# Kernel optimization log

Hardware: AMD Instinct MI355X
Metric: run time of the kernel (lower is better)

## Reference

```python
import jax, jax.numpy as jnp
import numpy as np

N = 10000        # nodes
E = 160000       # edges
C = 128          # channel multiplicity (128x0e input)
RBF = 20         # edge_attr_dim
HID = 32         # edge MLP hidden
WN = 3 * C       # tp.weight_numel: 3 uvu paths (0e x Y_l -> l), 128 weights each


def setup_inputs() -> dict:
    key = jax.random.key(0)
    ks = jax.random.split(key, 12)
    f = lambda k, s, sc=1.0: jax.random.normal(k, s, jnp.float32) * sc
    return {
        "node_feat": f(ks[0], (N, C)),
        "edge_attr": f(ks[1], (E, RBF)),
        "edge_rsh": f(ks[2], (E, 9)),
        "edge_index": jax.random.randint(ks[3], (2, E), 0, N),
        # mlp_edge_scalar: Linear(2C->32), Linear(32->WN)
        "Ws1": f(ks[4], (2 * C, HID), 1.0 / np.sqrt(2 * C)), "bs1": jnp.zeros((HID,), jnp.float32),
        "Ws2": f(ks[5], (HID, WN), 1.0 / np.sqrt(HID)), "bs2": jnp.zeros((WN,), jnp.float32),
        # mlp_edge_rbf: Linear(20->32), Linear(32->WN)
        "Wr1": f(ks[6], (RBF, HID), 1.0 / np.sqrt(RBF)), "br1": jnp.zeros((HID,), jnp.float32),
        "Wr2": f(ks[7], (HID, WN), 1.0 / np.sqrt(HID)), "br2": jnp.zeros((WN,), jnp.float32),
        "lin2_w0": f(ks[8], (C, C)), "lin2_b0": jnp.zeros((C,), jnp.float32),
        "lin2_w1": f(ks[9], (C, C)),
        "lin2_w2": f(ks[10], (C, C)),
    }


def reference(node_feat, edge_attr, edge_rsh, edge_index,
              Ws1, bs1, Ws2, bs2, Wr1, br1, Wr2, br2,
              lin2_w0, lin2_b0, lin2_w1, lin2_w2):
    src, dst = edge_index[0], edge_index[1]
    xi = node_feat[src]            # [E, C] gathered scalars (center node)
    xj = node_feat[dst]            # [E, C] gathered scalars (neighbor)

    # First-layer branch: inner_dot of pure scalars -> elementwise product;
    # slice [:, C:] is empty, so s0 = concat(x_i scalars, x_j scalars).
    s0 = jnp.concatenate([xi, xj], axis=-1)  # [E, 2C]

    silu = jax.nn.silu
    w_s = silu(s0 @ Ws1 + bs1) @ Ws2 + bs2            # [E, 3C]
    w_r = silu(edge_attr @ Wr1 + br1) @ Wr2 + br2      # [E, 3C]
    tpw = w_s * w_r                                    # gated tensor-product weights

    w0, w1, w2 = tpw[:, :C], tpw[:, C:2 * C], tpw[:, 2 * C:]
    y0, y1, y2 = edge_rsh[:, :1], edge_rsh[:, 1:4], edge_rsh[:, 4:9]

    # uvu tensor product: per edge, per channel u: w_l[u] * x[u] * Y_l[m]
    m0 = (w0 * xj) * y0                                        # [E, C]
    m1 = (w1 * xj)[:, :, None] * y1[:, None, :]                # [E, C, 3]
    m2 = (w2 * xj)[:, :, None] * y2[:, None, :]                # [E, C, 5]
    msg = jnp.concatenate(
        [m0, m1.reshape(-1, 3 * C), m2.reshape(-1, 5 * C)], axis=-1)  # [E, 9C]

    # scatter-add to destination (edge_index[0])
    accu = jax.ops.segment_sum(msg, src, num_segments=node_feat.shape[0])  # [N, 9C]

    # lin_node2: equivariant linear (per-l channel mixing, bias on scalars only)
    a0 = accu[:, :C]
    a1 = accu[:, C:4 * C].reshape(-1, C, 3)
    a2 = accu[:, 4 * C:].reshape(-1, C, 5)
    inv = 1.0 / np.sqrt(C)  # e3nn o3.Linear fan-in normalization
    o0 = a0 @ lin2_w0 * inv + lin2_b0
    o1 = jnp.einsum('ncm,cd->ndm', a1, lin2_w1) * inv
    o2 = jnp.einsum('ncm,cd->ndm', a2, lin2_w2) * inv
    return jnp.concatenate([o0, o1.reshape(-1, 3 * C), o2.reshape(-1, 5 * C)], axis=-1)
```

## Files before the change

kernel.cpp:

```cpp
#include <hip/hip_runtime.h>
#include <hip/hip_bf16.h>
#include <math.h>

#define NN   10000
#define EE   160000
#define CC   128
#define RBFD 20
#define HIDD 32
#define WND  384
#define MROW 1152
#define EPB  64

typedef _Float16 half2_t __attribute__((ext_vector_type(2)));

__device__ __forceinline__ half2_t u2h(unsigned int u)
{
    union { unsigned int u; half2_t h; } c; c.u = u; return c.h;
}
__device__ __forceinline__ unsigned int pack_h2(float a, float b)
{
    union { half2_t h; unsigned int u; } c;
    c.h.x = (_Float16)a; c.h.y = (_Float16)b; return c.u;
}

__device__ __align__(16) float g_proj[(size_t)NN * 64];
__device__ __align__(16) float g_accu[(size_t)NN * MROW];
__device__ __align__(16) uint4 g_wp[3 * 16 * 64];
__device__ int g_deg[NN];
__device__ int g_offs[NN + 1];
__device__ int g_rel[EE];
__device__ int g_ord[EE];

__device__ __forceinline__ float silu_f(float x) { return x / (1.f + __expf(-x)); }

__global__ __launch_bounds__(256) void zero_kernel()
{
    int tid = blockIdx.x * 256 + threadIdx.x;
    if (tid < NN) g_deg[tid] = 0;
    float4* p = reinterpret_cast<float4*>(g_accu);
    float4 z = make_float4(0.f, 0.f, 0.f, 0.f);
    int n4 = NN * MROW / 4;
    for (int i = tid; i < n4; i += gridDim.x * 256) p[i] = z;
}

__global__ __launch_bounds__(192) void pack_kernel(
    const float* __restrict__ Ws2, const float* __restrict__ Wr2)
{
    int tid = threadIdx.x;
    int sec = tid >> 6, l = tid & 63;
    int c0 = sec * 128 + 2 * l;
    #pragma unroll
    for (int q = 0; q < 4; ++q) {
        unsigned int w0[4], w1[4], r0[4], r1[4];
        #pragma unroll
        for (int i = 0; i < 4; ++i) {
            int p = 4 * q + i;
            int b0 = (2 * p) * WND + c0;
            int b1 = (2 * p + 1) * WND + c0;
            w0[i] = pack_h2(Ws2[b0],     Ws2[b1]);
            w1[i] = pack_h2(Ws2[b0 + 1], Ws2[b1 + 1]);
            r0[i] = pack_h2(Wr2[b0],     Wr2[b1]);
            r1[i] = pack_h2(Wr2[b0 + 1], Wr2[b1 + 1]);
        }
        g_wp[((sec * 16 + 0 * 4 + q) * 64) + l] = make_uint4(w0[0], w0[1], w0[2], w0[3]);
        g_wp[((sec * 16 + 1 * 4 + q) * 64) + l] = make_uint4(w1[0], w1[1], w1[2], w1[3]);
        g_wp[((sec * 16 + 2 * 4 + q) * 64) + l] = make_uint4(r0[0], r0[1], r0[2], r0[3]);
        g_wp[((sec * 16 + 3 * 4 + q) * 64) + l] = make_uint4(r1[0], r1[1], r1[2], r1[3]);
    }
}

__global__ __launch_bounds__(256) void hist_kernel(const int* __restrict__ edge_index)
{
    int e = blockIdx.x * 256 + threadIdx.x;
    if (e < EE) g_rel[e] = atomicAdd(&g_deg[edge_index[e]], 1);
}

__global__ __launch_bounds__(256) void scan_kernel()
{
    __shared__ int sP[256];
    int t = threadIdx.x;
    int lo = t * 40, hi = min(lo + 40, NN);
    int sum = 0;
    for (int i = lo; i < hi; ++i) sum += g_deg[i];
    sP[t] = sum;
    __syncthreads();
    for (int off = 1; off < 256; off <<= 1) {
        int v = (t >= off) ? sP[t - off] : 0;
        __syncthreads();
        sP[t] += v;
        __syncthreads();
    }
    int run = sP[t] - sum;
    if (t == 0) g_offs[0] = 0;
    for (int i = lo; i < hi; ++i) { run += g_deg[i]; g_offs[i + 1] = run; }
}

__global__ __launch_bounds__(256) void proj_kernel(
    const float* __restrict__ nf,
    const float* __restrict__ Ws1, const float* __restrict__ bs1,
    const int* __restrict__ edge_index)
{
    __shared__ float sX[16][132];

    int tid = threadIdx.x;
    int nb = blockIdx.x * 16;

    {
        int eg = blockIdx.x * 256 + tid;
        g_ord[g_offs[edge_index[eg]] + g_rel[eg]] = eg;
    }

    #pragma unroll
    for (int i = tid; i < 512; i += 256) {
        int n = i >> 5, k4 = i & 31;
        float4 v = reinterpret_cast<const float4*>(nf + (size_t)(nb + n) * CC)[k4];
        sX[n][k4 * 4 + 0] = v.x;
        sX[n][k4 * 4 + 1] = v.y;
        sX[n][k4 * 4 + 2] = v.z;
        sX[n][k4 * 4 + 3] = v.w;
    }
    __syncthreads();

    int nl = tid >> 4;
    int qd = tid & 15;
    int j0 = (qd & 7) * 4;
    int rbase = (qd >= 8) ? CC : 0;

    float4 acc;
    if (qd < 8) acc = *reinterpret_cast<const float4*>(&bs1[j0]);
    else        acc = make_float4(0.f, 0.f, 0.f, 0.f);

    const float* wb = Ws1 + (size_t)rbase * HIDD + j0;
    #pragma unroll 4
    for (int k = 0; k < CC; ++k) {
        float f = sX[nl][k];
        float4 w = *reinterpret_cast<const float4*>(wb + (size_t)k * HIDD);
        acc.x = fmaf(f, w.x, acc.x);
        acc.y = fmaf(f, w.y, acc.y);
        acc.z = fmaf(f, w.z, acc.z);
        acc.w = fmaf(f, w.w, acc.w);
    }

    float* o = g_proj + (size_t)(nb + nl) * 64 + ((qd >= 8) ? HIDD : 0) + j0;
    *reinterpret_cast<float4*>(o) = acc;
}

template<int K, int YB, int MOFF>
__device__ __forceinline__ void section_pass(
    int sec, int l,
    const float2* __restrict__ nf2,
    const float* __restrict__ bs2, const float* __restrict__ br2,
    const unsigned int (*__restrict__ sH)[36], const float (*__restrict__ sY)[9],
    const int* __restrict__ sSrc, const int* __restrict__ sDst)
{
    const uint4* wt = g_wp + (size_t)sec * 16 * 64 + l;
    uint4 W0q[4], W1q[4], R0q[4], R1q[4];
    #pragma unroll
    for (int q = 0; q < 4; ++q) {
        W0q[q] = wt[(0 * 4 + q) * 64];
        W1q[q] = wt[(1 * 4 + q) * 64];
        R0q[q] = wt[(2 * 4 + q) * 64];
        R1q[q] = wt[(3 * 4 + q) * 64];
    }

    float2 bsv = *reinterpret_cast<const float2*>(&bs2[sec * 128 + 2 * l]);
    float2 brv = *reinterpret_cast<const float2*>(&br2[sec * 128 + 2 * l]);

    float racc0[K], racc1[K];
    #pragma unroll
    for (int k = 0; k < K; ++k) { racc0[k] = 0.f; racc1[k] = 0.f; }
    int cur = sSrc[0];
    float2 xjn = nf2[(size_t)sDst[0] * 64 + l];

    #pragma unroll 2
    for (int ee = 0; ee < EPB; ++ee) {
        int src = sSrc[ee];
        if (src != cur) {
            float* ab = g_accu + (size_t)cur * MROW + MOFF + 2 * l;
            #pragma unroll
            for (int k = 0; k < K; ++k) {
                unsafeAtomicAdd(ab + k * CC,     racc0[k]);
                unsafeAtomicAdd(ab + k * CC + 1, racc1[k]);
                racc0[k] = 0.f; racc1[k] = 0.f;
            }
            cur = src;
        }
        float2 xj = xjn;
        xjn = nf2[(size_t)sDst[(ee + 1) & (EPB - 1)] * 64 + l];
        const uint4* hp = reinterpret_cast<const uint4*>(&sH[ee][0]);
        float as0 = bsv.x, as1 = bsv.y, ar0 = brv.x, ar1 = brv.y;
        #pragma unroll
        for (int q = 0; q < 4; ++q) {
            uint4 hv = hp[q];
            uint4 rv = hp[4 + q];
            as0 = __builtin_amdgcn_fdot2(u2h(hv.x), u2h(W0q[q].x), as0, false);
            as1 = __builtin_amdgcn_fdot2(u2h(hv.x), u2h(W1q[q].x), as1, false);
            as0 = __builtin_amdgcn_fdot2(u2h(hv.y), u2h(W0q[q].y), as0, false);
            as1 = __builtin_amdgcn_fdot2(u2h(hv.y), u2h(W1q[q].y), as1, false);
            as0 = __builtin_amdgcn_fdot2(u2h(hv.z), u2h(W0q[q].z), as0, false);
            as1 = __builtin_amdgcn_fdot2(u2h(hv.z), u2h(W1q[q].z), as1, false);
            as0 = __builtin_amdgcn_fdot2(u2h(hv.w), u2h(W0q[q].w), as0, false);
            as1 = __builtin_amdgcn_fdot2(u2h(hv.w), u2h(W1q[q].w), as1, false);
            ar0 = __builtin_amdgcn_fdot2(u2h(rv.x), u2h(R0q[q].x), ar0, false);
            ar1 = __builtin_amdgcn_fdot2(u2h(rv.x), u2h(R1q[q].x), ar1, false);
            ar0 = __builtin_amdgcn_fdot2(u2h(rv.y), u2h(R0q[q].y), ar0, false);
            ar1 = __builtin_amdgcn_fdot2(u2h(rv.y), u2h(R1q[q].y), ar1, false);
            ar0 = __builtin_amdgcn_fdot2(u2h(rv.z), u2h(R0q[q].z), ar0, false);
            ar1 = __builtin_amdgcn_fdot2(u2h(rv.z), u2h(R1q[q].z), ar1, false);
            ar0 = __builtin_amdgcn_fdot2(u2h(rv.w), u2h(R0q[q].w), ar0, false);
            ar1 = __builtin_amdgcn_fdot2(u2h(rv.w), u2h(R1q[q].w), ar1, false);
        }
        float u0 = as0 * ar0 * xj.x;
        float u1 = as1 * ar1 * xj.y;
        #pragma unroll
        for (int k = 0; k < K; ++k) {
            float yv = sY[ee][YB + k];
            racc0[k] = fmaf(u0, yv, racc0[k]);
            racc1[k] = fmaf(u1, yv, racc1[k]);
        }
    }
    float* ab = g_accu + (size_t)cur * MROW + MOFF + 2 * l;
    #pragma unroll
    for (int k = 0; k < K; ++k) {
        unsafeAtomicAdd(ab + k * CC,     racc0[k]);
        unsafeAtomicAdd(ab + k * CC + 1, racc1[k]);
    }
}

__global__ __launch_bounds__(192, 4) void fused_kernel(
    const float* __restrict__ nf,
    const float* __restrict__ edge_attr,
    const float* __restrict__ edge_rsh,
    const int*   __restrict__ edge_index,
    const float* __restrict__ bs2,
    const float* __restrict__ Wr1, const float* __restrict__ br1,
    const float* __restrict__ br2)
{
    __shared__ unsigned int sH[EPB][36];
    __shared__ float sY[EPB][9];
    __shared__ int   sSrc[EPB], sDst[EPB];

    int tid = threadIdx.x;
    int w = tid / 64;
    int l = tid & 63;
    int p = blockIdx.x * EPB + l;
    int e = g_ord[p];

    if (w == 0) {
        int s = edge_index[e];
        int t = edge_index[EE + e];
        const float4* pi = reinterpret_cast<const float4*>(g_proj + (size_t)s * 64);
        const float4* pj = reinterpret_cast<const float4*>(g_proj + (size_t)t * 64 + HIDD);
        #pragma unroll
        for (int j4 = 0; j4 < HIDD / 8; ++j4) {
            float4 a0 = pi[2 * j4],     b0 = pj[2 * j4];
            float4 a1 = pi[2 * j4 + 1], b1 = pj[2 * j4 + 1];
            sH[l][4 * j4 + 0] = pack_h2(silu_f(a0.x + b0.x), silu_f(a0.y + b0.y));
            sH[l][4 * j4 + 1] = pack_h2(silu_f(a0.z + b0.z), silu_f(a0.w + b0.w));
            sH[l][4 * j4 + 2] = pack_h2(silu_f(a1.x + b1.x), silu_f(a1.y + b1.y));
            sH[l][4 * j4 + 3] = pack_h2(silu_f(a1.z + b1.z), silu_f(a1.w + b1.w));
        }
        sSrc[l] = s;
        sDst[l] = t;
    } else if (w == 1) {
        float hr[HIDD];
        #pragma unroll
        for (int j = 0; j < HIDD; ++j) hr[j] = br1[j];
        #pragma unroll 1
        for (int k4 = 0; k4 < RBFD / 4; ++k4) {
            float4 a = reinterpret_cast<const float4*>(edge_attr + (size_t)e * RBFD)[k4];
            const float* wp = Wr1 + (4 * k4) * HIDD;
            #pragma unroll
            for (int j = 0; j < HIDD; ++j) {
                hr[j] = fmaf(a.x, wp[j], hr[j]);
                hr[j] = fmaf(a.y, wp[HIDD + j], hr[j]);
                hr[j] = fmaf(a.z, wp[2 * HIDD + j], hr[j]);
                hr[j] = fmaf(a.w, wp[3 * HIDD + j], hr[j]);
            }
        }
        #pragma unroll
        for (int pp = 0; pp < 16; ++pp)
            sH[l][16 + pp] = pack_h2(silu_f(hr[2 * pp]), silu_f(hr[2 * pp + 1]));
    } else {
        #pragma unroll
        for (int i = 0; i < 9; ++i) sY[l][i] = edge_rsh[(size_t)e * 9 + i];
    }
    __syncthreads();

    const float2* nf2 = reinterpret_cast<const float2*>(nf);
    if (w == 0)
        section_pass<1, 0, 0>     (0, l, nf2, bs2, br2, sH, sY, sSrc, sDst);
    else if (w == 1)
        section_pass<3, 1, CC>    (1, l, nf2, bs2, br2, sH, sY, sSrc, sDst);
    else
        section_pass<5, 4, 4 * CC>(2, l, nf2, bs2, br2, sH, sY, sSrc, sDst);
}

__global__ __launch_bounds__(256) void lin2_kernel(
    const float* __restrict__ W0, const float* __restrict__ b0,
    const float* __restrict__ W1, const float* __restrict__ W2,
    float* __restrict__ out)
{
    __shared__ float sA[8 * MROW];
    int n0 = blockIdx.x * 8;
    const float4* g = reinterpret_cast<const float4*>(g_accu + (size_t)n0 * MROW);
    for (int i = threadIdx.x; i < 8 * MROW / 4; i += 256)
        reinterpret_cast<float4*>(sA)[i] = g[i];
    __syncthreads();

    int d  = threadIdx.x & (CC - 1);
    int nl = threadIdx.x >> 7;

    float acc[4][9];
    #pragma unroll
    for (int q = 0; q < 4; ++q)
        #pragma unroll
        for (int m = 0; m < 9; ++m) acc[q][m] = 0.f;

    #pragma unroll 1
    for (int c = 0; c < CC; ++c) {
        float w0 = W0[c * CC + d];
        float w1 = W1[c * CC + d];
        float w2 = W2[c * CC + d];
        #pragma unroll
        for (int q = 0; q < 4; ++q) {
            const float* a = sA + (size_t)(nl * 4 + q) * MROW;
            acc[q][0] = fmaf(a[c],          w0, acc[q][0]);
            acc[q][1] = fmaf(a[CC + c],     w1, acc[q][1]);
            acc[q][2] = fmaf(a[2 * CC + c], w1, acc[q][2]);
            acc[q][3] = fmaf(a[3 * CC + c], w1, acc[q][3]);
            acc[q][4] = fmaf(a[4 * CC + c], w2, acc[q][4]);
            acc[q][5] = fmaf(a[5 * CC + c], w2, acc[q][5]);
            acc[q][6] = fmaf(a[6 * CC + c], w2, acc[q][6]);
            acc[q][7] = fmaf(a[7 * CC + c], w2, acc[q][7]);
            acc[q][8] = fmaf(a[8 * CC + c], w2, acc[q][8]);
        }
    }

    const float inv = 0.08838834764831845f;
    #pragma unroll
    for (int q = 0; q < 4; ++q) {
        size_t ob = (size_t)(n0 + nl * 4 + q) * MROW;
        out[ob + d] = acc[q][0] * inv + b0[d];
        #pragma unroll
        for (int m = 0; m < 3; ++m) out[ob + CC + d * 3 + m]     = acc[q][1 + m] * inv;
        #pragma unroll
        for (int m = 0; m < 5; ++m) out[ob + 4 * CC + d * 5 + m] = acc[q][4 + m] * inv;
    }
}

extern "C" void kernel_launch(void* const* d_in, const int* in_sizes, int n_in,
                              void* d_out, int out_size, void* d_ws, size_t ws_size,
                              hipStream_t stream)
{
    const float* node_feat  = (const float*)d_in[0];
    const float* edge_attr  = (const float*)d_in[1];
    const float* edge_rsh   = (const float*)d_in[2];
    const int*   edge_index = (const int*)  d_in[3];
    const float* Ws1 = (const float*)d_in[4];
    const float* bs1 = (const float*)d_in[5];
    const float* Ws2 = (const float*)d_in[6];
    const float* bs2 = (const float*)d_in[7];
    const float* Wr1 = (const float*)d_in[8];
    const float* br1 = (const float*)d_in[9];
    const float* Wr2 = (const float*)d_in[10];
    const float* br2 = (const float*)d_in[11];
    const float* W0  = (const float*)d_in[12];
    const float* b0  = (const float*)d_in[13];
    const float* W1  = (const float*)d_in[14];
    const float* W2  = (const float*)d_in[15];
    float* out = (float*)d_out;

    zero_kernel<<<2048, 256, 0, stream>>>();
    pack_kernel<<<1, 192, 0, stream>>>(Ws2, Wr2);
    hist_kernel<<<EE / 256, 256, 0, stream>>>(edge_index);
    scan_kernel<<<1, 256, 0, stream>>>();
    proj_kernel<<<NN / 16, 256, 0, stream>>>(node_feat, Ws1, bs1, edge_index);
    fused_kernel<<<EE / EPB, 192, 0, stream>>>(
        node_feat, edge_attr, edge_rsh, edge_index,
        bs2, Wr1, br1, br2);
    lin2_kernel<<<NN / 8, 256, 0, stream>>>(W0, b0, W1, W2, out);
}
```

Measured before the change: 283.7 us.

## Zero accumulator inside lin2, tile edges by four, vectorize lin2 LDS reads

Drops the separate zero kernel. The degree array is now cleared in pack_kernel, and lin2_kernel writes zeros back to the accumulator rows after copying them into shared memory, so the buffer is clean for the next call. The fused edge kernel processes four edges per step and reloads the packed fp16 MLP weights from global memory for each group, instead of keeping them in registers for the whole block. This lowers register pressure and gives more independent dot-product chains. lin2 now reads the accumulator from LDS as float4 and unrolls the channel loop by four; the zeroing trick depends on lin2 always running after every fused pass.

New measurement: 991.1 us. 3.49x slower.

```diff
diff --git a/kernel.cpp b/kernel.cpp
--- a/kernel.cpp
+++ b/kernel.cpp
@@ -10,6 +10,7 @@
 #define WND  384
 #define MROW 1152
 #define EPB  64
+#define ET   4
 
 typedef _Float16 half2_t __attribute__((ext_vector_type(2)));
 
@@ -33,20 +34,11 @@
 
 __device__ __forceinline__ float silu_f(float x) { return x / (1.f + __expf(-x)); }
 
-__global__ __launch_bounds__(256) void zero_kernel()
-{
-    int tid = blockIdx.x * 256 + threadIdx.x;
-    if (tid < NN) g_deg[tid] = 0;
-    float4* p = reinterpret_cast<float4*>(g_accu);
-    float4 z = make_float4(0.f, 0.f, 0.f, 0.f);
-    int n4 = NN * MROW / 4;
-    for (int i = tid; i < n4; i += gridDim.x * 256) p[i] = z;
-}
-
 __global__ __launch_bounds__(192) void pack_kernel(
     const float* __restrict__ Ws2, const float* __restrict__ Wr2)
 {
     int tid = threadIdx.x;
+    for (int i = tid; i < NN; i += 192) g_deg[i] = 0;
     int sec = tid >> 6, l = tid & 63;
     int c0 = sec * 128 + 2 * l;
     #pragma unroll
@@ -154,15 +146,6 @@
     const int* __restrict__ sSrc, const int* __restrict__ sDst)
 {
     const uint4* wt = g_wp + (size_t)sec * 16 * 64 + l;
-    uint4 W0q[4], W1q[4], R0q[4], R1q[4];
-    #pragma unroll
-    for (int q = 0; q < 4; ++q) {
-        W0q[q] = wt[(0 * 4 + q) * 64];
-        W1q[q] = wt[(1 * 4 + q) * 64];
-        R0q[q] = wt[(2 * 4 + q) * 64];
-        R1q[q] = wt[(3 * 4 + q) * 64];
-    }
-
     float2 bsv = *reinterpret_cast<const float2*>(&bs2[sec * 128 + 2 * l]);
     float2 brv = *reinterpret_cast<const float2*>(&br2[sec * 128 + 2 * l]);
 
@@ -170,53 +153,71 @@
     #pragma unroll
     for (int k = 0; k < K; ++k) { racc0[k] = 0.f; racc1[k] = 0.f; }
     int cur = sSrc[0];
-    float2 xjn = nf2[(size_t)sDst[0] * 64 + l];
-
-    #pragma unroll 2
-    for (int ee = 0; ee < EPB; ++ee) {
-        int src = sSrc[ee];
-        if (src != cur) {
-            float* ab = g_accu + (size_t)cur * MROW + MOFF + 2 * l;
+
+    #pragma unroll 1
+    for (int et = 0; et < EPB / ET; ++et) {
+        float2 xjv[ET];
+        #pragma unroll
+        for (int e4 = 0; e4 < ET; ++e4)
+            xjv[e4] = nf2[(size_t)sDst[et * ET + e4] * 64 + l];
+
+        float as0[ET], as1[ET], ar0[ET], ar1[ET];
+        #pragma unroll
+        for (int e4 = 0; e4 < ET; ++e4) {
+            as0[e4] = bsv.x; as1[e4] = bsv.y;
+            ar0[e4] = brv.x; ar1[e4] = brv.y;
+        }
+        #pragma unroll
+        for (int q = 0; q < 4; ++q) {
+            uint4 w0q = wt[(0 * 4 + q) * 64];
+            uint4 w1q = wt[(1 * 4 + q) * 64];
+            uint4 r0q = wt[(2 * 4 + q) * 64];
+            uint4 r1q = wt[(3 * 4 + q) * 64];
+            #pragma unroll
+            for (int e4 = 0; e4 < ET; ++e4) {
+                const uint4* hp = reinterpret_cast<const uint4*>(&sH[et * ET + e4][0]);
+                uint4 hv = hp[q];
+                uint4 rv = hp[4 + q];
+                as0[e4] = __builtin_amdgcn_fdot2(u2h(hv.x), u2h(w0q.x), as0[e4], false);
+                as1[e4] = __builtin_amdgcn_fdot2(u2h(hv.x), u2h(w1q.x), as1[e4], false);
+                as0[e4] = __builtin_amdgcn_fdot2(u2h(hv.y), u2h(w0q.y), as0[e4], false);
+                as1[e4] = __builtin_amdgcn_fdot2(u2h(hv.y), u2h(w1q.y), as1[e4], false);
+                as0[e4] = __builtin_amdgcn_fdot2(u2h(hv.z), u2h(w0q.z), as0[e4], false);
+                as1[e4] = __builtin_amdgcn_fdot2(u2h(hv.z), u2h(w1q.z), as1[e4], false);
+                as0[e4] = __builtin_amdgcn_fdot2(u2h(hv.w), u2h(w0q.w), as0[e4], false);
+                as1[e4] = __builtin_amdgcn_fdot2(u2h(hv.w), u2h(w1q.w), as1[e4], false);
+                ar0[e4] = __builtin_amdgcn_fdot2(u2h(rv.x), u2h(r0q.x), ar0[e4], false);
+                ar1[e4] = __builtin_amdgcn_fdot2(u2h(rv.x), u2h(r1q.x), ar1[e4], false);
+                ar0[e4] = __builtin_amdgcn_fdot2(u2h(rv.y), u2h(r0q.y), ar0[e4], false);
+                ar1[e4] = __builtin_amdgcn_fdot2(u2h(rv.y), u2h(r1q.y), ar1[e4], false);
+                ar0[e4] = __builtin_amdgcn_fdot2(u2h(rv.z), u2h(r0q.z), ar0[e4], false);
+                ar1[e4] = __builtin_amdgcn_fdot2(u2h(rv.z), u2h(r1q.z), ar1[e4], false);
+                ar0[e4] = __builtin_amdgcn_fdot2(u2h(rv.w), u2h(r0q.w), ar0[e4], false);
+                ar1[e4] = __builtin_amdgcn_fdot2(u2h(rv.w), u2h(r1q.w), ar1[e4], false);
+            }
+        }
+        #pragma unroll
+        for (int e4 = 0; e4 < ET; ++e4) {
+            int idx = et * ET + e4;
+            int src = sSrc[idx];
+            if (src != cur) {
+                float* ab = g_accu + (size_t)cur * MROW + MOFF + 2 * l;
+                #pragma unroll
+                for (int k = 0; k < K; ++k) {
+                    unsafeAtomicAdd(ab + k * CC,     racc0[k]);
+                    unsafeAtomicAdd(ab + k * CC + 1, racc1[k]);
+                    racc0[k] = 0.f; racc1[k] = 0.f;
+                }
+                cur = src;
+            }
+            float u0 = as0[e4] * ar0[e4] * xjv[e4].x;
+            float u1 = as1[e4] * ar1[e4] * xjv[e4].y;
             #pragma unroll
             for (int k = 0; k < K; ++k) {
-                unsafeAtomicAdd(ab + k * CC,     racc0[k]);
-                unsafeAtomicAdd(ab + k * CC + 1, racc1[k]);
-                racc0[k] = 0.f; racc1[k] = 0.f;
-            }
-            cur = src;
-        }
-        float2 xj = xjn;
-        xjn = nf2[(size_t)sDst[(ee + 1) & (EPB - 1)] * 64 + l];
-        const uint4* hp = reinterpret_cast<const uint4*>(&sH[ee][0]);
-        float as0 = bsv.x, as1 = bsv.y, ar0 = brv.x, ar1 = brv.y;
-        #pragma unroll
-        for (int q = 0; q < 4; ++q) {
-            uint4 hv = hp[q];
-            uint4 rv = hp[4 + q];
-            as0 = __builtin_amdgcn_fdot2(u2h(hv.x), u2h(W0q[q].x), as0, false);
-            as1 = __builtin_amdgcn_fdot2(u2h(hv.x), u2h(W1q[q].x), as1, false);
-            as0 = __builtin_amdgcn_fdot2(u2h(hv.y), u2h(W0q[q].y), as0, false);
-            as1 = __builtin_amdgcn_fdot2(u2h(hv.y), u2h(W1q[q].y), as1, false);
-            as0 = __builtin_amdgcn_fdot2(u2h(hv.z), u2h(W0q[q].z), as0, false);
-            as1 = __builtin_amdgcn_fdot2(u2h(hv.z), u2h(W1q[q].z), as1, false);
-            as0 = __builtin_amdgcn_fdot2(u2h(hv.w), u2h(W0q[q].w), as0, false);
-            as1 = __builtin_amdgcn_fdot2(u2h(hv.w), u2h(W1q[q].w), as1, false);
-            ar0 = __builtin_amdgcn_fdot2(u2h(rv.x), u2h(R0q[q].x), ar0, false);
-            ar1 = __builtin_amdgcn_fdot2(u2h(rv.x), u2h(R1q[q].x), ar1, false);
-            ar0 = __builtin_amdgcn_fdot2(u2h(rv.y), u2h(R0q[q].y), ar0, false);
-            ar1 = __builtin_amdgcn_fdot2(u2h(rv.y), u2h(R1q[q].y), ar1, false);
-            ar0 = __builtin_amdgcn_fdot2(u2h(rv.z), u2h(R0q[q].z), ar0, false);
-            ar1 = __builtin_amdgcn_fdot2(u2h(rv.z), u2h(R1q[q].z), ar1, false);
-            ar0 = __builtin_amdgcn_fdot2(u2h(rv.w), u2h(R0q[q].w), ar0, false);
-            ar1 = __builtin_amdgcn_fdot2(u2h(rv.w), u2h(R1q[q].w), ar1, false);
-        }
-        float u0 = as0 * ar0 * xj.x;
-        float u1 = as1 * ar1 * xj.y;
-        #pragma unroll
-        for (int k = 0; k < K; ++k) {
-            float yv = sY[ee][YB + k];
-            racc0[k] = fmaf(u0, yv, racc0[k]);
-            racc1[k] = fmaf(u1, yv, racc1[k]);
+                float yv = sY[idx][YB + k];
+                racc0[k] = fmaf(u0, yv, racc0[k]);
+                racc1[k] = fmaf(u1, yv, racc1[k]);
+            }
         }
     }
     float* ab = g_accu + (size_t)cur * MROW + MOFF + 2 * l;
@@ -303,9 +304,13 @@
 {
     __shared__ float sA[8 * MROW];
     int n0 = blockIdx.x * 8;
-    const float4* g = reinterpret_cast<const float4*>(g_accu + (size_t)n0 * MROW);
-    for (int i = threadIdx.x; i < 8 * MROW / 4; i += 256)
-        reinterpret_cast<float4*>(sA)[i] = g[i];
+    float4* g = reinterpret_cast<float4*>(g_accu + (size_t)n0 * MROW);
+    const float4 z4 = make_float4(0.f, 0.f, 0.f, 0.f);
+    for (int i = threadIdx.x; i < 8 * MROW / 4; i += 256) {
+        float4 v = g[i];
+        reinterpret_cast<float4*>(sA)[i] = v;
+        g[i] = z4;
+    }
     __syncthreads();
 
     int d  = threadIdx.x & (CC - 1);
@@ -318,22 +323,33 @@
         for (int m = 0; m < 9; ++m) acc[q][m] = 0.f;
 
     #pragma unroll 1
-    for (int c = 0; c < CC; ++c) {
-        float w0 = W0[c * CC + d];
-        float w1 = W1[c * CC + d];
-        float w2 = W2[c * CC + d];
+    for (int c4 = 0; c4 < CC / 4; ++c4) {
+        float w0c[4], w1c[4], w2c[4];
+        #pragma unroll
+        for (int cc = 0; cc < 4; ++cc) {
+            int c = 4 * c4 + cc;
+            w0c[cc] = W0[c * CC + d];
+            w1c[cc] = W1[c * CC + d];
+            w2c[cc] = W2[c * CC + d];
+        }
         #pragma unroll
         for (int q = 0; q < 4; ++q) {
-            const float* a = sA + (size_t)(nl * 4 + q) * MROW;
-            acc[q][0] = fmaf(a[c],          w0, acc[q][0]);
-            acc[q][1] = fmaf(a[CC + c],     w1, acc[q][1]);
-            acc[q][2] = fmaf(a[2 * CC + c], w1, acc[q][2]);
-            acc[q][3] = fmaf(a[3 * CC + c], w1, acc[q][3]);
-            acc[q][4] = fmaf(a[4 * CC + c], w2, acc[q][4]);
-            acc[q][5] = fmaf(a[5 * CC + c], w2, acc[q][5]);
-            acc[q][6] = fmaf(a[6 * CC + c], w2, acc[q][6]);
-            acc[q][7] = fmaf(a[7 * CC + c], w2, acc[q][7]);
-            acc[q][8] = fmaf(a[8 * CC + c], w2, acc[q][8]);
+            const float* a = sA + (size_t)(nl * 4 + q) * MROW + 4 * c4;
+            float4 am[9];
+            #pragma unroll
+            for (int m = 0; m < 9; ++m)
+                am[m] = *reinterpret_cast<const float4*>(a + m * CC);
+            #pragma unroll
+            for (int cc = 0; cc < 4; ++cc) {
+                float a0 = (&am[0].x)[cc];
+                acc[q][0] = fmaf(a0, w0c[cc], acc[q][0]);
+                #pragma unroll
+                for (int m = 1; m < 4; ++m)
+                    acc[q][m] = fmaf((&am[m].x)[cc], w1c[cc], acc[q][m]);
+                #pragma unroll
+                for (int m = 4; m < 9; ++m)
+                    acc[q][m] = fmaf((&am[m].x)[cc], w2c[cc], acc[q][m]);
+            }
         }
     }
 
@@ -371,7 +387,6 @@
     const float* W2  = (const float*)d_in[15];
     float* out = (float*)d_out;
 
-    zero_kernel<<<2048, 256, 0, stream>>>();
     pack_kernel<<<1, 192, 0, stream>>>(Ws2, Wr2);
     hist_kernel<<<EE / 256, 256, 0, stream>>>(edge_index);
     scan_kernel<<<1, 256, 0, stream>>>();
```
